# Optimization experiments

Hardware: AMD Instinct MI355X
Metric: run time of the kernel (lower is better)

## Reference

```python
import jax, jax.numpy as jnp
import numpy as np

N = 50000   # nodes
E = 800000  # edges (avg degree 16)
D = 64      # in = hidden = out channels, head = 1


def _linear_params(key, d_in, d_out):
    kw, kb = jax.random.split(key)
    scale = 1.0 / np.sqrt(d_in)
    W = jax.random.uniform(kw, (d_in, d_out), jnp.float32, -scale, scale)
    b = jax.random.uniform(kb, (d_out,), jnp.float32, -scale, scale)
    return W, b


def _tconv(x, src, dst, Wq, bq, Wk, bk, Wv, bv, Ws, bs):
    """PyG TransformerConv, heads=1, concat=True, root_weight=True."""
    n = x.shape[0]
    d = Wq.shape[1]
    q = x @ Wq + bq  # [N, d] query at target
    k = x @ Wk + bk  # [N, d] key at source
    v = x @ Wv + bv  # [N, d] value at source
    # per-edge attention logits: (q_i . k_j) / sqrt(d)
    scores = jnp.einsum('ed,ed->e', q[dst], k[src]) / jnp.sqrt(jnp.asarray(d, x.dtype))
    # segment softmax over incoming edges of each target node
    m = jax.ops.segment_max(scores, dst, num_segments=n)
    ex = jnp.exp(scores - m[dst])
    denom = jax.ops.segment_sum(ex, dst, num_segments=n)
    agg = jax.ops.segment_sum(ex[:, None] * v[src], dst, num_segments=n)
    denom_safe = jnp.where(denom > 0, denom, 1.0)  # guard isolated nodes
    return agg / denom_safe[:, None] + (x @ Ws + bs)  # + skip (root weight)


def setup_inputs() -> dict:
    key = jax.random.key(0)
    keys = jax.random.split(key, 32)
    inp = {
        'x': jax.random.normal(keys[0], (N, D), jnp.float32),
        'edge_index': jax.random.randint(keys[1], (2, E), 0, N, jnp.int64),
        'z': jax.random.normal(keys[2], (N, D), jnp.float32),
    }
    ki = 3
    for l in (1, 2, 3):
        for nm in ('q', 'k', 'v', 's'):
            W, b = _linear_params(keys[ki], D, D)
            ki += 1
            inp[f'W{nm}{l}'] = W
            inp[f'b{nm}{l}'] = b
    return inp


def reference(x, edge_index, z,
              Wq1, bq1, Wk1, bk1, Wv1, bv1, Ws1, bs1,
              Wq2, bq2, Wk2, bk2, Wv2, bv2, Ws2, bs2,
              Wq3, bq3, Wk3, bk3, Wv3, bv3, Ws3, bs3):
    src, dst = edge_index[0], edge_index[1]
    h = jax.nn.silu(_tconv(x, src, dst, Wq1, bq1, Wk1, bk1, Wv1, bv1, Ws1, bs1))
    h = jax.nn.silu(_tconv(h, src, dst, Wq2, bq2, Wk2, bk2, Wv2, bv2, Ws2, bs2) + h)
    drift = _tconv(h, src, dst, Wq3, bq3, Wk3, bk3, Wv3, bv3, Ws3, bs3)
    std, sqrt_d = 0.01, 0.1
    return drift + std * z / sqrt_d
```

## Files before the change

kernel.cpp:

```cpp
#include <hip/hip_runtime.h>
#include <math.h>


#define D64 64
#define KVF 64
#define NPB 128
#define MAXNB 512
#define CHUNK 4096

typedef _Float16 h2 __attribute__((ext_vector_type(2)));
typedef __attribute__((ext_vector_type(8))) short bf16x8;
typedef __attribute__((ext_vector_type(4))) float f32x4;
typedef unsigned int uint32;

__device__ __forceinline__ unsigned short bf16_rne(float f) {
    unsigned int u = __float_as_uint(f);
    u += 0x7FFFu + ((u >> 16) & 1u);
    return (unsigned short)(u >> 16);
}

__global__ void detect_fmt(const int* __restrict__ ei, int nchecks, int* flag) {
    int t = blockIdx.x * blockDim.x + threadIdx.x;
    int acc = 0;
    for (int i = t; i < nchecks; i += blockDim.x * gridDim.x)
        acc |= ei[2 * i + 1];
    if (acc) atomicOr(flag, 1);
}

__device__ __forceinline__ int load_src(const int* ei, int e, int E, int is64) {
    return is64 ? ei[2 * e] : ei[e];
}
__device__ __forceinline__ int load_dst(const int* ei, int e, int E, int is64) {
    return is64 ? ei[2 * E + 2 * e] : ei[E + e];
}

__global__ void bucket_hist(const int* __restrict__ ei, int* __restrict__ bhT,
                            int E, int nblk, int NB, const int* __restrict__ flag) {
    __shared__ int h[MAXNB];
    int blk = blockIdx.x, tid = threadIdx.x;
    for (int i = tid; i < NB; i += 256) h[i] = 0;
    __syncthreads();
    int is64 = (*flag == 0);
    int e1 = blk * CHUNK + CHUNK; if (e1 > E) e1 = E;
    for (int e = blk * CHUNK + tid; e < e1; e += 256)
        atomicAdd(&h[load_dst(ei, e, E, is64) >> 7], 1);
    __syncthreads();
    for (int i = tid; i < NB; i += 256) bhT[i * nblk + blk] = h[i];
}

__global__ void scan_blocks(const int* __restrict__ counts, int* __restrict__ partial,
                            int* __restrict__ blockSums, int n) {
    int tid = threadIdx.x;
    int base = blockIdx.x * 1024 + tid * 4;
    int4 c = make_int4(0, 0, 0, 0);
    if (base + 3 < n) c = *(const int4*)&counts[base];
    else {
        if (base + 0 < n) c.x = counts[base + 0];
        if (base + 1 < n) c.y = counts[base + 1];
        if (base + 2 < n) c.z = counts[base + 2];
        if (base + 3 < n) c.w = counts[base + 3];
    }
    int s1 = c.x, s2 = s1 + c.y, s3 = s2 + c.z, s4 = s3 + c.w;
    int lane = tid & 63, wave = tid >> 6;
    int v = s4;
#pragma unroll
    for (int off = 1; off < 64; off <<= 1) {
        int t = __shfl_up(v, off);
        if (lane >= off) v += t;
    }
    __shared__ int wsum[4];
    if (lane == 63) wsum[wave] = v;
    __syncthreads();
    int wpre = 0;
    for (int w = 0; w < wave; ++w) wpre += wsum[w];
    int pre = wpre + v - s4;
    if (base + 0 < n) partial[base + 0] = pre + s1;
    if (base + 1 < n) partial[base + 1] = pre + s2;
    if (base + 2 < n) partial[base + 2] = pre + s3;
    if (base + 3 < n) partial[base + 3] = pre + s4;
    if (tid == 255) blockSums[blockIdx.x] = wsum[0] + wsum[1] + wsum[2] + wsum[3];
}

__global__ void scan_sums(int* __restrict__ bs, int nb) {
    int lane = threadIdx.x;
    int carry = 0;
    for (int b0 = 0; b0 < nb; b0 += 64) {
        int i = b0 + lane;
        int val = (i < nb) ? bs[i] : 0;
        int v = val;
#pragma unroll
        for (int off = 1; off < 64; off <<= 1) {
            int t = __shfl_up(v, off);
            if (lane >= off) v += t;
        }
        if (i < nb) bs[i] = carry + v - val;
        carry += __shfl(v, 63);
    }
}

__global__ void make_excl(const int* __restrict__ bh, const int* __restrict__ partial,
                          const int* __restrict__ bs, int* __restrict__ ebase, int n) {
    int i = blockIdx.x * 256 + threadIdx.x;
    if (i >= n) return;
    ebase[i] = partial[i] + bs[i >> 10] - bh[i];
}

__global__ void bucket_scatter(const int* __restrict__ ei, const int* __restrict__ ebase,
                               int2* __restrict__ pairs, int E, int nblk, int NB,
                               const int* __restrict__ flag) {
    __shared__ int cur[MAXNB];
    int blk = blockIdx.x, tid = threadIdx.x;
    for (int i = tid; i < NB; i += 256) cur[i] = ebase[i * nblk + blk];
    __syncthreads();
    int is64 = (*flag == 0);
    int e1 = blk * CHUNK + CHUNK; if (e1 > E) e1 = E;
    for (int e = blk * CHUNK + tid; e < e1; e += 256) {
        int s = load_src(ei, e, E, is64);
        int d = load_dst(ei, e, E, is64);
        int pos = atomicAdd(&cur[d >> 7], 1);
        pairs[pos] = make_int2(s, d);
    }
}

__global__ void bucket_finalize(const int2* __restrict__ pairs,
                                const int* __restrict__ ebase, int nblk, int NB,
                                int* __restrict__ csr_src, int* __restrict__ offsets,
                                int N, int E) {
    __shared__ int hist[NPB];
    __shared__ int cur[NPB];
    int b = blockIdx.x, tid = threadIdx.x;
    int n0 = b * NPB;
    int cnt = N - n0; if (cnt > NPB) cnt = NPB;
    if (cnt <= 0) return;
    int estart = ebase[b * nblk];
    int eend = (b + 1 < NB) ? ebase[(b + 1) * nblk] : E;
    for (int i = tid; i < cnt; i += 256) hist[i] = 0;
    __syncthreads();
    for (int e = estart + tid; e < eend; e += 256)
        atomicAdd(&hist[pairs[e].y - n0], 1);
    __syncthreads();
    if (tid == 0) {
        int run = estart;
        for (int i = 0; i < cnt; ++i) {
            cur[i] = run;
            offsets[n0 + i] = run;
            run += hist[i];
        }
    }
    if (b == 0 && tid == 1) offsets[N] = E;
    __syncthreads();
    for (int e = estart + tid; e < eend; e += 256) {
        int2 pr = pairs[e];
        int pos = atomicAdd(&cur[pr.y - n0], 1);
        csr_src[pos] = pr.x;
    }
}

__global__ void prep_w(const float* W0, const float* W1, const float* W2,
                       const float* W3, const float* W4, const float* W5,
                       const float* W6, const float* W7, const float* W8,
                       const float* W9, const float* W10, const float* W11,
                       uint32* __restrict__ wpack) {
    const float* Wm;
    switch (blockIdx.x) {
        case 0: Wm = W0; break;  case 1: Wm = W1; break;
        case 2: Wm = W2; break;  case 3: Wm = W3; break;
        case 4: Wm = W4; break;  case 5: Wm = W5; break;
        case 6: Wm = W6; break;  case 7: Wm = W7; break;
        case 8: Wm = W8; break;  case 9: Wm = W9; break;
        case 10: Wm = W10; break; default: Wm = W11; break;
    }
    int layer = blockIdx.x >> 2, mat = blockIdx.x & 3;
    uint32* hiB = wpack + layer * 16384;
    uint32* loB = hiB + 8192;
    int d = threadIdx.x & 63;
    int cg = threadIdx.x >> 6;
    int col = mat * 64 + d;
    for (int kw = cg; kw < 32; kw += 4) {
        float w0 = Wm[(2 * kw) * 64 + d];
        float w1 = Wm[(2 * kw + 1) * 64 + d];
        unsigned short h0 = bf16_rne(w0);
        unsigned short h1 = bf16_rne(w1);
        float r0 = w0 - __uint_as_float(((uint32)h0) << 16);
        float r1 = w1 - __uint_as_float(((uint32)h1) << 16);
        unsigned short l0 = bf16_rne(r0);
        unsigned short l1 = bf16_rne(r1);
        int sw = ((kw * 4) ^ ((col & 7) << 4)) >> 2;
        hiB[col * 32 + sw] = (uint32)h0 | ((uint32)h1 << 16);
        loB[col * 32 + sw] = (uint32)l0 | ((uint32)l1 << 16);
    }
}

__launch_bounds__(256)
__global__ void gemm_mfma(const float* __restrict__ x, const uint32* __restrict__ wpackL,
                          const float* __restrict__ bq, const float* __restrict__ bk,
                          const float* __restrict__ bv, const float* __restrict__ bs,
                          float* __restrict__ q, float* __restrict__ kv,
                          float* __restrict__ s, int n) {
    __shared__ uint32 wlds[16384];
    int tid = threadIdx.x;
#pragma unroll
    for (int r = 0; r < 16; ++r) {
        int w4 = r * 1024 + tid * 4;
        *(uint4*)&wlds[w4] = *(const uint4*)&wpackL[w4];
    }
    __syncthreads();

    int lane = tid & 63, wave = tid >> 6;
    int row0 = blockIdx.x * 64 + wave * 16;
    int arow = row0 + (lane & 15);
    int kgrp = (lane >> 4) * 8;
    bool rowok = arow < n;
    const float* xr = x + (size_t)(rowok ? arow : 0) * D64;

    bf16x8 ahi[2], alo[2];
#pragma unroll
    for (int st = 0; st < 2; ++st) {
        float4 xa = rowok ? *(const float4*)(xr + st * 32 + kgrp)
                          : make_float4(0.f, 0.f, 0.f, 0.f);
        float4 xb = rowok ? *(const float4*)(xr + st * 32 + kgrp + 4)
                          : make_float4(0.f, 0.f, 0.f, 0.f);
        float xs[8] = {xa.x, xa.y, xa.z, xa.w, xb.x, xb.y, xb.z, xb.w};
#pragma unroll
        for (int j = 0; j < 8; ++j) {
            unsigned short h = bf16_rne(xs[j]);
            float rem = xs[j] - __uint_as_float(((uint32)h) << 16);
            ahi[st][j] = (short)h;
            alo[st][j] = (short)bf16_rne(rem);
        }
    }

    f32x4 acc[16];
#pragma unroll
    for (int t = 0; t < 16; ++t) acc[t] = f32x4{0.f, 0.f, 0.f, 0.f};

#pragma unroll
    for (int t = 0; t < 16; ++t) {
        int col = t * 16 + (lane & 15);
#pragma unroll
        for (int st = 0; st < 2; ++st) {
            int kidx = st * 32 + kgrp;
            int boff = col * 128 + ((kidx * 2) ^ ((col & 7) << 4));
            bf16x8 bhi = *(const bf16x8*)((const char*)wlds + boff);
            bf16x8 blo = *(const bf16x8*)((const char*)wlds + boff + 32768);
            acc[t] = __builtin_amdgcn_mfma_f32_16x16x32_bf16(alo[st], bhi, acc[t], 0, 0, 0);
            acc[t] = __builtin_amdgcn_mfma_f32_16x16x32_bf16(ahi[st], blo, acc[t], 0, 0, 0);
            acc[t] = __builtin_amdgcn_mfma_f32_16x16x32_bf16(ahi[st], bhi, acc[t], 0, 0, 0);
        }
    }

    int drow0 = row0 + (lane >> 4) * 4;
    int c16 = lane & 15;
#pragma unroll
    for (int t = 0; t < 4; ++t) {
        float bb = bq[t * 16 + c16];
#pragma unroll
        for (int r = 0; r < 4; ++r) {
            int row = drow0 + r;
            if (row < n) q[(size_t)row * D64 + t * 16 + c16] = acc[t][r] + bb;
        }
    }
#pragma unroll
    for (int t = 0; t < 4; ++t) {
        float bb = bs[t * 16 + c16];
#pragma unroll
        for (int r = 0; r < 4; ++r) {
            int row = drow0 + r;
            if (row < n) s[(size_t)row * D64 + t * 16 + c16] = acc[12 + t][r] + bb;
        }
    }
#pragma unroll
    for (int t = 0; t < 4; ++t) {
        float bkk = bk[t * 16 + c16];
        float bvv = bv[t * 16 + c16];
        int c = t * 16 + c16;
#pragma unroll
        for (int r = 0; r < 4; ++r) {
            int row = drow0 + r;
            float kval = acc[4 + t][r] + bkk;
            float vval = acc[8 + t][r] + bvv;
            uint32 kh = (uint32)__builtin_bit_cast(unsigned short, (_Float16)kval);
            uint32 kp = (uint32)__shfl_xor((int)kh, 1);
            uint32 kword = (lane & 1) ? (kp | (kh << 16)) : (kh | (kp << 16));
            uint32 vh = (uint32)bf16_rne(vval);
            uint32 vp = (uint32)__shfl_xor((int)vh, 1);
            uint32 vword = (lane & 1) ? (vp | (vh << 16)) : (vh | (vp << 16));
            if (row < n && !(lane & 1)) {
                uint32* rowp = (uint32*)(kv + (size_t)row * KVF);
                rowp[c >> 1] = kword;
                rowp[32 + (c >> 1)] = vword;
            }
        }
    }
}

template <int MODE>
__launch_bounds__(256)
__global__ void agg_fused(const float* __restrict__ q, const float* __restrict__ kv,
                          const int* __restrict__ csr_src,
                          const int* __restrict__ offsets,
                          const float* __restrict__ sbuf, const float* __restrict__ xin,
                          const float* __restrict__ z, float* __restrict__ out, int n) {
    int node = blockIdx.x * 4 + (threadIdx.x >> 6);
    if (node >= n) return;
    int lane = threadIdx.x & 63;
    int grp = lane >> 3, l8 = lane & 7;
    int start = offsets[node], end = offsets[node + 1];
    size_t co = (size_t)node * D64 + l8 * 8;
    float4 ta = *(const float4*)(sbuf + co);
    float4 tb = *(const float4*)(sbuf + co + 4);

    if (end > start) {
        const float4 qa = *(const float4*)(q + co);
        const float4 qb = *(const float4*)(q + co + 4);
        h2 hq0, hq1, hq2, hq3;
        hq0[0] = (_Float16)qa.x; hq0[1] = (_Float16)qa.y;
        hq1[0] = (_Float16)qa.z; hq1[1] = (_Float16)qa.w;
        hq2[0] = (_Float16)qb.x; hq2[1] = (_Float16)qb.y;
        hq3[0] = (_Float16)qb.z; hq3[1] = (_Float16)qb.w;
        float m = -3.0e38f, den = 0.f;
        float4 aa = make_float4(0.f, 0.f, 0.f, 0.f);
        float4 ab = make_float4(0.f, 0.f, 0.f, 0.f);

        int i = start + grp;
        int idx0 = (i < end) ? i : start;
        int sj0 = csr_src[idx0];
        const float* kp0 = kv + (size_t)sj0 * KVF;
        float4 kw = *(const float4*)(kp0 + l8 * 4);
        float4 vw = *(const float4*)(kp0 + 32 + l8 * 4);

        while (i < end) {
            int inext = i + 8;
            int idx1 = (inext < end) ? inext : start;
            int sj1 = csr_src[idx1];
            const float* kp1 = kv + (size_t)sj1 * KVF;
            float4 kw1 = *(const float4*)(kp1 + l8 * 4);
            float4 vw1 = *(const float4*)(kp1 + 32 + l8 * 4);

            float p = __builtin_amdgcn_fdot2(hq0, __builtin_bit_cast(h2, kw.x),
                                             0.f, false);
            p = __builtin_amdgcn_fdot2(hq1, __builtin_bit_cast(h2, kw.y), p, false);
            p = __builtin_amdgcn_fdot2(hq2, __builtin_bit_cast(h2, kw.z), p, false);
            p = __builtin_amdgcn_fdot2(hq3, __builtin_bit_cast(h2, kw.w), p, false);
            p += __shfl_xor(p, 1, 8);
            p += __shfl_xor(p, 2, 8);
            p += __shfl_xor(p, 4, 8);
            p *= 0.125f;
            float nm = fmaxf(m, p);
            float f  = __expf(m - nm);
            float e  = __expf(p - nm);
            den = den * f + e;
            unsigned int u0 = __float_as_uint(vw.x), u1 = __float_as_uint(vw.y);
            unsigned int u2 = __float_as_uint(vw.z), u3 = __float_as_uint(vw.w);
            float v0 = __uint_as_float(u0 << 16), v1 = __uint_as_float(u0 & 0xFFFF0000u);
            float v2 = __uint_as_float(u1 << 16), v3 = __uint_as_float(u1 & 0xFFFF0000u);
            float v4 = __uint_as_float(u2 << 16), v5 = __uint_as_float(u2 & 0xFFFF0000u);
            float v6 = __uint_as_float(u3 << 16), v7 = __uint_as_float(u3 & 0xFFFF0000u);
            aa.x = aa.x * f + e * v0; aa.y = aa.y * f + e * v1;
            aa.z = aa.z * f + e * v2; aa.w = aa.w * f + e * v3;
            ab.x = ab.x * f + e * v4; ab.y = ab.y * f + e * v5;
            ab.z = ab.z * f + e * v6; ab.w = ab.w * f + e * v7;
            m = nm;
            kw = kw1; vw = vw1;
            i = inext;
        }
        float M = fmaxf(m, __shfl_xor(m, 8));
        M = fmaxf(M, __shfl_xor(M, 16));
        M = fmaxf(M, __shfl_xor(M, 32));
        float f = __expf(m - M);
        float dd = den * f;
        dd += __shfl_xor(dd, 8); dd += __shfl_xor(dd, 16); dd += __shfl_xor(dd, 32);
        aa.x *= f; aa.y *= f; aa.z *= f; aa.w *= f;
        ab.x *= f; ab.y *= f; ab.z *= f; ab.w *= f;
        aa.x += __shfl_xor(aa.x, 8); aa.x += __shfl_xor(aa.x, 16); aa.x += __shfl_xor(aa.x, 32);
        aa.y += __shfl_xor(aa.y, 8); aa.y += __shfl_xor(aa.y, 16); aa.y += __shfl_xor(aa.y, 32);
        aa.z += __shfl_xor(aa.z, 8); aa.z += __shfl_xor(aa.z, 16); aa.z += __shfl_xor(aa.z, 32);
        aa.w += __shfl_xor(aa.w, 8); aa.w += __shfl_xor(aa.w, 16); aa.w += __shfl_xor(aa.w, 32);
        ab.x += __shfl_xor(ab.x, 8); ab.x += __shfl_xor(ab.x, 16); ab.x += __shfl_xor(ab.x, 32);
        ab.y += __shfl_xor(ab.y, 8); ab.y += __shfl_xor(ab.y, 16); ab.y += __shfl_xor(ab.y, 32);
        ab.z += __shfl_xor(ab.z, 8); ab.z += __shfl_xor(ab.z, 16); ab.z += __shfl_xor(ab.z, 32);
        ab.w += __shfl_xor(ab.w, 8); ab.w += __shfl_xor(ab.w, 16); ab.w += __shfl_xor(ab.w, 32);
        float inv = 1.f / dd;
        ta.x += aa.x * inv; ta.y += aa.y * inv; ta.z += aa.z * inv; ta.w += aa.w * inv;
        tb.x += ab.x * inv; tb.y += ab.y * inv; tb.z += ab.z * inv; tb.w += ab.w * inv;
    }
    if (MODE == 1) {
        ta.x = ta.x / (1.f + __expf(-ta.x)); ta.y = ta.y / (1.f + __expf(-ta.y));
        ta.z = ta.z / (1.f + __expf(-ta.z)); ta.w = ta.w / (1.f + __expf(-ta.w));
        tb.x = tb.x / (1.f + __expf(-tb.x)); tb.y = tb.y / (1.f + __expf(-tb.y));
        tb.z = tb.z / (1.f + __expf(-tb.z)); tb.w = tb.w / (1.f + __expf(-tb.w));
    } else if (MODE == 2) {
        const float4 xa = *(const float4*)(xin + co);
        const float4 xb = *(const float4*)(xin + co + 4);
        float u;
        u = ta.x + xa.x; ta.x = u / (1.f + __expf(-u));
        u = ta.y + xa.y; ta.y = u / (1.f + __expf(-u));
        u = ta.z + xa.z; ta.z = u / (1.f + __expf(-u));
        u = ta.w + xa.w; ta.w = u / (1.f + __expf(-u));
        u = tb.x + xb.x; tb.x = u / (1.f + __expf(-u));
        u = tb.y + xb.y; tb.y = u / (1.f + __expf(-u));
        u = tb.z + xb.z; tb.z = u / (1.f + __expf(-u));
        u = tb.w + xb.w; tb.w = u / (1.f + __expf(-u));
    } else {
        const float4 za = *(const float4*)(z + co);
        const float4 zb = *(const float4*)(z + co + 4);
        ta.x += 0.1f * za.x; ta.y += 0.1f * za.y;
        ta.z += 0.1f * za.z; ta.w += 0.1f * za.w;
        tb.x += 0.1f * zb.x; tb.y += 0.1f * zb.y;
        tb.z += 0.1f * zb.z; tb.w += 0.1f * zb.w;
    }
    if (grp == 0) {
        *(float4*)(out + co) = ta;
        *(float4*)(out + co + 4) = tb;
    }
}

extern "C" void kernel_launch(void* const* d_in, const int* in_sizes, int n_in,
                              void* d_out, int out_size, void* d_ws, size_t ws_size,
                              hipStream_t stream) {
    const float* x = (const float*)d_in[0];
    const int* ei  = (const int*)d_in[1];
    const float* z = (const float*)d_in[2];
    const float* W[3][4];
    const float* B[3][4];
    for (int l = 0; l < 3; ++l)
        for (int m = 0; m < 4; ++m) {
            W[l][m] = (const float*)d_in[3 + l * 8 + m * 2];
            B[l][m] = (const float*)d_in[3 + l * 8 + m * 2 + 1];
        }
    int N = in_sizes[0] / D64;
    int E = in_sizes[1] / 2;
    size_t ND = (size_t)N * D64;

    int NB   = (N + NPB - 1) / NPB;
    int nblk = (E + CHUNK - 1) / CHUNK;
    int nscan = NB * nblk;
    int nb2  = (nscan + 1023) / 1024;

    char* p = (char*)d_ws;
    auto alloc = [&](size_t bytes) {
        char* r = p;
        p += (bytes + 255) & ~(size_t)255;
        return r;
    };
    float* q       = (float*)alloc(ND * 4);
    float* kv      = (float*)alloc((size_t)N * KVF * 4);
    float* sb      = (float*)alloc(ND * 4);
    float* hA      = (float*)alloc(ND * 4);
    int* csr_src   = (int*)alloc((size_t)E * 4);
    int2* pairs    = (int2*)alloc((size_t)E * 8);
    int* offsets   = (int*)alloc((size_t)(N + 1) * 4);
    int* bhT       = (int*)alloc((size_t)nscan * 4);
    int* partial   = (int*)alloc((size_t)nscan * 4);
    int* ebase     = (int*)alloc((size_t)nscan * 4);
    int* blockSums = (int*)alloc((size_t)nb2 * 4);
    uint32* wpack  = (uint32*)alloc(3 * 16384 * 4);
    int* flag      = (int*)alloc(4);
    float* outp    = (float*)d_out;

    hipMemsetAsync(flag, 0, 4, stream);
    int nchecks = E < 4096 ? E : 4096;
    detect_fmt<<<1, 256, 0, stream>>>(ei, nchecks, flag);
    prep_w<<<12, 256, 0, stream>>>(W[0][0], W[0][1], W[0][2], W[0][3],
                                   W[1][0], W[1][1], W[1][2], W[1][3],
                                   W[2][0], W[2][1], W[2][2], W[2][3], wpack);
    bucket_hist<<<nblk, 256, 0, stream>>>(ei, bhT, E, nblk, NB, flag);
    scan_blocks<<<nb2, 256, 0, stream>>>(bhT, partial, blockSums, nscan);
    scan_sums<<<1, 64, 0, stream>>>(blockSums, nb2);
    make_excl<<<(nscan + 255) / 256, 256, 0, stream>>>(bhT, partial, blockSums,
                                                       ebase, nscan);
    bucket_scatter<<<nblk, 256, 0, stream>>>(ei, ebase, pairs, E, nblk, NB, flag);
    bucket_finalize<<<NB, 256, 0, stream>>>(pairs, ebase, nblk, NB,
                                            csr_src, offsets, N, E);

    int gemm_grid = (N + 63) / 64;
    int node_grid = (N + 3) / 4;

    gemm_mfma<<<gemm_grid, 256, 0, stream>>>(x, wpack, B[0][0], B[0][1],
                                             B[0][2], B[0][3], q, kv, sb, N);
    agg_fused<1><<<node_grid, 256, 0, stream>>>(q, kv, csr_src, offsets, sb,
                                                nullptr, nullptr, hA, N);
    gemm_mfma<<<gemm_grid, 256, 0, stream>>>(hA, wpack + 16384, B[1][0], B[1][1],
                                             B[1][2], B[1][3], q, kv, sb, N);
    agg_fused<2><<<node_grid, 256, 0, stream>>>(q, kv, csr_src, offsets, sb,
                                                hA, nullptr, hA, N);
    gemm_mfma<<<gemm_grid, 256, 0, stream>>>(hA, wpack + 32768, B[2][0], B[2][1],
                                             B[2][2], B[2][3], q, kv, sb, N);
    agg_fused<3><<<node_grid, 256, 0, stream>>>(q, kv, csr_src, offsets, sb,
                                                nullptr, z, outp, N);
}
```

Before: 239.1 us.

## Pack edge pairs into 32-bit words and use fast exp/rcp intrinsics

New measurement: 235.2 us. No clear change (-1.6%).

```diff
diff --git a/kernel.cpp b/kernel.cpp
--- a/kernel.cpp
+++ b/kernel.cpp
@@ -17,6 +17,12 @@
     unsigned int u = __float_as_uint(f);
     u += 0x7FFFu + ((u >> 16) & 1u);
     return (unsigned short)(u >> 16);
+}
+__device__ __forceinline__ float fexp(float x) {
+    return __builtin_amdgcn_exp2f(x * 1.44269504089f);
+}
+__device__ __forceinline__ float frcp(float x) {
+    return __builtin_amdgcn_rcpf(x);
 }
 
 __global__ void detect_fmt(const int* __restrict__ ei, int nchecks, int* flag) {
@@ -34,16 +40,21 @@
     return is64 ? ei[2 * E + 2 * e] : ei[E + e];
 }
 
-__global__ void bucket_hist(const int* __restrict__ ei, int* __restrict__ bhT,
-                            int E, int nblk, int NB, const int* __restrict__ flag) {
+__global__ void hist_pack(const int* __restrict__ ei, int* __restrict__ bhT,
+                          uint32* __restrict__ pc, int E, int nblk, int NB,
+                          const int* __restrict__ flag) {
     __shared__ int h[MAXNB];
     int blk = blockIdx.x, tid = threadIdx.x;
     for (int i = tid; i < NB; i += 256) h[i] = 0;
     __syncthreads();
     int is64 = (*flag == 0);
     int e1 = blk * CHUNK + CHUNK; if (e1 > E) e1 = E;
-    for (int e = blk * CHUNK + tid; e < e1; e += 256)
-        atomicAdd(&h[load_dst(ei, e, E, is64) >> 7], 1);
+    for (int e = blk * CHUNK + tid; e < e1; e += 256) {
+        int s = load_src(ei, e, E, is64);
+        int d = load_dst(ei, e, E, is64);
+        pc[e] = (uint32)s | ((uint32)d << 16);
+        atomicAdd(&h[d >> 7], 1);
+    }
     __syncthreads();
     for (int i = tid; i < NB; i += 256) bhT[i * nblk + blk] = h[i];
 }
@@ -105,24 +116,21 @@
     ebase[i] = partial[i] + bs[i >> 10] - bh[i];
 }
 
-__global__ void bucket_scatter(const int* __restrict__ ei, const int* __restrict__ ebase,
-                               int2* __restrict__ pairs, int E, int nblk, int NB,
-                               const int* __restrict__ flag) {
+__global__ void bucket_scatter(const uint32* __restrict__ pc, const int* __restrict__ ebase,
+                               uint32* __restrict__ pairs, int E, int nblk, int NB) {
     __shared__ int cur[MAXNB];
     int blk = blockIdx.x, tid = threadIdx.x;
     for (int i = tid; i < NB; i += 256) cur[i] = ebase[i * nblk + blk];
     __syncthreads();
-    int is64 = (*flag == 0);
     int e1 = blk * CHUNK + CHUNK; if (e1 > E) e1 = E;
     for (int e = blk * CHUNK + tid; e < e1; e += 256) {
-        int s = load_src(ei, e, E, is64);
-        int d = load_dst(ei, e, E, is64);
-        int pos = atomicAdd(&cur[d >> 7], 1);
-        pairs[pos] = make_int2(s, d);
-    }
-}
-
-__global__ void bucket_finalize(const int2* __restrict__ pairs,
+        uint32 w = pc[e];
+        int pos = atomicAdd(&cur[w >> 23], 1);
+        pairs[pos] = w;
+    }
+}
+
+__global__ void bucket_finalize(const uint32* __restrict__ pairs,
                                 const int* __restrict__ ebase, int nblk, int NB,
                                 int* __restrict__ csr_src, int* __restrict__ offsets,
                                 int N, int E) {
@@ -137,7 +145,7 @@
     for (int i = tid; i < cnt; i += 256) hist[i] = 0;
     __syncthreads();
     for (int e = estart + tid; e < eend; e += 256)
-        atomicAdd(&hist[pairs[e].y - n0], 1);
+        atomicAdd(&hist[(int)(pairs[e] >> 16) - n0], 1);
     __syncthreads();
     if (tid == 0) {
         int run = estart;
@@ -150,9 +158,9 @@
     if (b == 0 && tid == 1) offsets[N] = E;
     __syncthreads();
     for (int e = estart + tid; e < eend; e += 256) {
-        int2 pr = pairs[e];
-        int pos = atomicAdd(&cur[pr.y - n0], 1);
-        csr_src[pos] = pr.x;
+        uint32 w = pairs[e];
+        int pos = atomicAdd(&cur[(int)(w >> 16) - n0], 1);
+        csr_src[pos] = (int)(w & 0xFFFFu);
     }
 }
 
@@ -314,10 +322,10 @@
         const float4 qa = *(const float4*)(q + co);
         const float4 qb = *(const float4*)(q + co + 4);
         h2 hq0, hq1, hq2, hq3;
-        hq0[0] = (_Float16)qa.x; hq0[1] = (_Float16)qa.y;
-        hq1[0] = (_Float16)qa.z; hq1[1] = (_Float16)qa.w;
-        hq2[0] = (_Float16)qb.x; hq2[1] = (_Float16)qb.y;
-        hq3[0] = (_Float16)qb.z; hq3[1] = (_Float16)qb.w;
+        hq0[0] = (_Float16)(qa.x * 0.125f); hq0[1] = (_Float16)(qa.y * 0.125f);
+        hq1[0] = (_Float16)(qa.z * 0.125f); hq1[1] = (_Float16)(qa.w * 0.125f);
+        hq2[0] = (_Float16)(qb.x * 0.125f); hq2[1] = (_Float16)(qb.y * 0.125f);
+        hq3[0] = (_Float16)(qb.z * 0.125f); hq3[1] = (_Float16)(qb.w * 0.125f);
         float m = -3.0e38f, den = 0.f;
         float4 aa = make_float4(0.f, 0.f, 0.f, 0.f);
         float4 ab = make_float4(0.f, 0.f, 0.f, 0.f);
@@ -345,10 +353,9 @@
             p += __shfl_xor(p, 1, 8);
             p += __shfl_xor(p, 2, 8);
             p += __shfl_xor(p, 4, 8);
-            p *= 0.125f;
             float nm = fmaxf(m, p);
-            float f  = __expf(m - nm);
-            float e  = __expf(p - nm);
+            float f  = fexp(m - nm);
+            float e  = fexp(p - nm);
             den = den * f + e;
             unsigned int u0 = __float_as_uint(vw.x), u1 = __float_as_uint(vw.y);
             unsigned int u2 = __float_as_uint(vw.z), u3 = __float_as_uint(vw.w);
@@ -367,7 +374,7 @@
         float M = fmaxf(m, __shfl_xor(m, 8));
         M = fmaxf(M, __shfl_xor(M, 16));
         M = fmaxf(M, __shfl_xor(M, 32));
-        float f = __expf(m - M);
+        float f = fexp(m - M);
         float dd = den * f;
         dd += __shfl_xor(dd, 8); dd += __shfl_xor(dd, 16); dd += __shfl_xor(dd, 32);
         aa.x *= f; aa.y *= f; aa.z *= f; aa.w *= f;
@@ -380,27 +387,27 @@
         ab.y += __shfl_xor(ab.y, 8); ab.y += __shfl_xor(ab.y, 16); ab.y += __shfl_xor(ab.y, 32);
         ab.z += __shfl_xor(ab.z, 8); ab.z += __shfl_xor(ab.z, 16); ab.z += __shfl_xor(ab.z, 32);
         ab.w += __shfl_xor(ab.w, 8); ab.w += __shfl_xor(ab.w, 16); ab.w += __shfl_xor(ab.w, 32);
-        float inv = 1.f / dd;
+        float inv = frcp(dd);
         ta.x += aa.x * inv; ta.y += aa.y * inv; ta.z += aa.z * inv; ta.w += aa.w * inv;
         tb.x += ab.x * inv; tb.y += ab.y * inv; tb.z += ab.z * inv; tb.w += ab.w * inv;
     }
     if (MODE == 1) {
-        ta.x = ta.x / (1.f + __expf(-ta.x)); ta.y = ta.y / (1.f + __expf(-ta.y));
-        ta.z = ta.z / (1.f + __expf(-ta.z)); ta.w = ta.w / (1.f + __expf(-ta.w));
-        tb.x = tb.x / (1.f + __expf(-tb.x)); tb.y = tb.y / (1.f + __expf(-tb.y));
-        tb.z = tb.z / (1.f + __expf(-tb.z)); tb.w = tb.w / (1.f + __expf(-tb.w));
+        ta.x *= frcp(1.f + fexp(-ta.x)); ta.y *= frcp(1.f + fexp(-ta.y));
+        ta.z *= frcp(1.f + fexp(-ta.z)); ta.w *= frcp(1.f + fexp(-ta.w));
+        tb.x *= frcp(1.f + fexp(-tb.x)); tb.y *= frcp(1.f + fexp(-tb.y));
+        tb.z *= frcp(1.f + fexp(-tb.z)); tb.w *= frcp(1.f + fexp(-tb.w));
     } else if (MODE == 2) {
         const float4 xa = *(const float4*)(xin + co);
         const float4 xb = *(const float4*)(xin + co + 4);
         float u;
-        u = ta.x + xa.x; ta.x = u / (1.f + __expf(-u));
-        u = ta.y + xa.y; ta.y = u / (1.f + __expf(-u));
-        u = ta.z + xa.z; ta.z = u / (1.f + __expf(-u));
-        u = ta.w + xa.w; ta.w = u / (1.f + __expf(-u));
-        u = tb.x + xb.x; tb.x = u / (1.f + __expf(-u));
-        u = tb.y + xb.y; tb.y = u / (1.f + __expf(-u));
-        u = tb.z + xb.z; tb.z = u / (1.f + __expf(-u));
-        u = tb.w + xb.w; tb.w = u / (1.f + __expf(-u));
+        u = ta.x + xa.x; ta.x = u * frcp(1.f + fexp(-u));
+        u = ta.y + xa.y; ta.y = u * frcp(1.f + fexp(-u));
+        u = ta.z + xa.z; ta.z = u * frcp(1.f + fexp(-u));
+        u = ta.w + xa.w; ta.w = u * frcp(1.f + fexp(-u));
+        u = tb.x + xb.x; tb.x = u * frcp(1.f + fexp(-u));
+        u = tb.y + xb.y; tb.y = u * frcp(1.f + fexp(-u));
+        u = tb.z + xb.z; tb.z = u * frcp(1.f + fexp(-u));
+        u = tb.w + xb.w; tb.w = u * frcp(1.f + fexp(-u));
     } else {
         const float4 za = *(const float4*)(z + co);
         const float4 zb = *(const float4*)(z + co + 4);
@@ -448,7 +455,8 @@
     float* sb      = (float*)alloc(ND * 4);
     float* hA      = (float*)alloc(ND * 4);
     int* csr_src   = (int*)alloc((size_t)E * 4);
-    int2* pairs    = (int2*)alloc((size_t)E * 8);
+    uint32* pc     = (uint32*)alloc((size_t)E * 4);
+    uint32* pairs  = (uint32*)alloc((size_t)E * 4);
     int* offsets   = (int*)alloc((size_t)(N + 1) * 4);
     int* bhT       = (int*)alloc((size_t)nscan * 4);
     int* partial   = (int*)alloc((size_t)nscan * 4);
@@ -464,12 +472,12 @@
     prep_w<<<12, 256, 0, stream>>>(W[0][0], W[0][1], W[0][2], W[0][3],
                                    W[1][0], W[1][1], W[1][2], W[1][3],
                                    W[2][0], W[2][1], W[2][2], W[2][3], wpack);
-    bucket_hist<<<nblk, 256, 0, stream>>>(ei, bhT, E, nblk, NB, flag);
+    hist_pack<<<nblk, 256, 0, stream>>>(ei, bhT, pc, E, nblk, NB, flag);
     scan_blocks<<<nb2, 256, 0, stream>>>(bhT, partial, blockSums, nscan);
     scan_sums<<<1, 64, 0, stream>>>(blockSums, nb2);
     make_excl<<<(nscan + 255) / 256, 256, 0, stream>>>(bhT, partial, blockSums,
                                                        ebase, nscan);
-    bucket_scatter<<<nblk, 256, 0, stream>>>(ei, ebase, pairs, E, nblk, NB, flag);
+    bucket_scatter<<<nblk, 256, 0, stream>>>(pc, ebase, pairs, E, nblk, NB);
     bucket_finalize<<<NB, 256, 0, stream>>>(pairs, ebase, nblk, NB,
                                             csr_src, offsets, N, E);
 
```
